# Optimization experiments

Measured on AMD Instinct MI355X. Metric: run time of the kernel, lower is better.

The kernel has to match this reference:

```python
import jax, jax.numpy as jnp
import numpy as np

B, S, H, HKV, D = 4, 1024, 32, 8, 128   # batch segments, seq per segment, q heads, kv heads, head dim
N = B * S                                # Ntotal (ragged tokens, equal-length segments)
SCALE = 1.0 / np.sqrt(D)                 # softmax_scale init kwarg
NEG = -1e9


def setup_inputs() -> dict:
    key = jax.random.key(0)
    kq, kk, kv = jax.random.split(key, 3)
    q = jax.random.normal(kq, (N, H, D), jnp.float32)
    k = jax.random.normal(kk, (N, HKV, D), jnp.float32)
    v = jax.random.normal(kv, (N, HKV, D), jnp.float32)
    # RoPE angles, rotate-half convention: concat(freqs, freqs), broadcast over heads
    inv_freq = 1.0 / (10000.0 ** (jnp.arange(D // 2, dtype=jnp.float32) / (D // 2)))
    pos = jnp.arange(S, dtype=jnp.float32)
    ang = pos[:, None] * inv_freq[None, :]                      # [S, D/2]
    idx_theta = jnp.tile(jnp.concatenate([ang, ang], -1), (B, 1))[:, None, :]  # [N,1,D]
    # per-segment causal mask, stacked -> [N, S]
    causal = jnp.where(jnp.arange(S)[None, :] <= jnp.arange(S)[:, None], 0.0, NEG).astype(jnp.float32)
    mask = jnp.tile(causal, (B, 1))
    return {"q": q, "k": k, "v": v, "idx_theta": idx_theta, "mask": mask}


def _rotate_half(x):
    # cat(-x[..., D/2:], x[..., :D/2])
    return jnp.concatenate([-x[..., D // 2:], x[..., : D // 2]], axis=-1)


def reference(q, k, v, idx_theta, mask):
    rep = H // HKV
    # repeat_kv: attention head i uses kv head i // rep (matches torch expand+reshape order)
    kx = jnp.repeat(k, rep, axis=1)                    # [N, H, D]
    vx = jnp.repeat(v, rep, axis=1)
    cos, sin = jnp.cos(idx_theta), jnp.sin(idx_theta)
    qr = q * cos + _rotate_half(q) * sin
    kr = kx * cos + _rotate_half(kx) * sin
    # segment-blocked attention (equal-length segments, vectorized over batch & heads)
    qb = qr.reshape(B, S, H, D)
    kb = kr.reshape(B, S, H, D)
    vb = vx.reshape(B, S, H, D)
    mb = mask.reshape(B, S, S)[:, None, :, :]          # [B,1,S,S]
    scores = jnp.einsum('bqhd,bkhd->bhqk', qb, kb) * SCALE + mb
    l = jax.nn.logsumexp(scores, axis=-1)              # [B,H,S] == max + logsumexp(shifted)
    p = jax.nn.softmax(scores, axis=-1)
    o = jnp.einsum('bhqk,bkhd->bqhd', p, vb)           # [B,S,H,D]
    o = o.reshape(N, H * D)                            # o.reshape(Ntotal, num_head, -1) flattened last two in torch is (N,H,D)->(N,H,D); original reshape(q.shape[0], q.shape[1], -1) keeps [N,H,D]
    o = o.reshape(N, H, D)
    l = l.transpose(0, 2, 1).reshape(N, H, 1)          # [Ntotal, num_head, 1]
    return o, l
```

## Files before the change

kernel.cpp:

```cpp
#include <hip/hip_runtime.h>

#define B_    4
#define S_    1024
#define H_    32
#define HKV_  8
#define D_    128
#define NTOT  (B_*S_)
#define QT_   64
#define KT_   64
#define DPAD  (D_+8)
#define KPAD  (KT_+8)

#define SCALE_ 0.08838834764831845f

typedef __attribute__((ext_vector_type(8))) short bf16x8;
typedef __attribute__((ext_vector_type(4))) short bf16x4;
typedef __attribute__((ext_vector_type(4))) float f32x4;
typedef __attribute__((ext_vector_type(4))) int   int4v;

__device__ __forceinline__ unsigned short f2bf(float f) {
    unsigned int u = __float_as_uint(f);
    u += 0x7FFFu + ((u >> 16) & 1u);
    return (unsigned short)(u >> 16);
}
__device__ __forceinline__ unsigned int pack2bf(float a, float b) {
    return (unsigned int)f2bf(a) | ((unsigned int)f2bf(b) << 16);
}

__global__ void rope_k_kernel(const float* __restrict__ k,
                              const float* __restrict__ theta,
                              unsigned short* __restrict__ kr) {
    int t  = blockIdx.x * blockDim.x + threadIdx.x;
    int g  = t & 7;
    int hk = (t >> 3) & (HKV_ - 1);
    int n  = t >> 6;
    if (n >= NTOT) return;
    int d0 = g * 8;
    const float* kp = k + ((size_t)n * HKV_ + hk) * D_;
    const float* tp = theta + (size_t)n * D_;

    alignas(16) float kl[8], ku[8], thl[8], thu[8];
    *(float4*)&kl[0]  = *(const float4*)(kp + d0);
    *(float4*)&kl[4]  = *(const float4*)(kp + d0 + 4);
    *(float4*)&ku[0]  = *(const float4*)(kp + d0 + 64);
    *(float4*)&ku[4]  = *(const float4*)(kp + d0 + 68);
    *(float4*)&thl[0] = *(const float4*)(tp + d0);
    *(float4*)&thl[4] = *(const float4*)(tp + d0 + 4);
    *(float4*)&thu[0] = *(const float4*)(tp + d0 + 64);
    *(float4*)&thu[4] = *(const float4*)(tp + d0 + 68);

    alignas(16) unsigned short ol[8], ou[8];
#pragma unroll
    for (int j = 0; j < 8; ++j) {
        float sl, cl, su, cu;
        __sincosf(thl[j], &sl, &cl);
        __sincosf(thu[j], &su, &cu);
        ol[j] = f2bf(kl[j] * cl - ku[j] * sl);
        ou[j] = f2bf(ku[j] * cu + kl[j] * su);
    }
    unsigned short* outp = kr + ((size_t)n * HKV_ + hk) * D_;
    *(int4v*)(outp + d0)      = *(const int4v*)ol;
    *(int4v*)(outp + d0 + 64) = *(const int4v*)ou;
}

__global__ void vt_kernel(const float* __restrict__ v,
                          unsigned short* __restrict__ vt) {
    __shared__ unsigned short T[64][128];
    int blk = blockIdx.x;
    int s0  = (blk & (S_/64 - 1)) * 64;
    int hk  = (blk >> 4) & (HKV_ - 1);
    int b   = blk >> 7;
    int tid = threadIdx.x;

#pragma unroll
    for (int i = 0; i < 8; ++i) {
        int u  = tid + 256 * i;
        int s  = u >> 5;
        int G  = u & 31;
        float4 val = *(const float4*)(v + (((size_t)(b * S_ + s0 + s)) * HKV_ + hk) * D_ + G * 4);
        unsigned short* p = &T[s][(G ^ (s & 31)) * 4];
        p[0] = f2bf(val.x); p[1] = f2bf(val.y); p[2] = f2bf(val.z); p[3] = f2bf(val.w);
    }
    __syncthreads();
#pragma unroll
    for (int i = 0; i < 4; ++i) {
        int u = tid + 256 * i;
        int d = u >> 3;
        int g = u & 7;
        int G = d >> 2;
        alignas(16) unsigned short tmp[8];
#pragma unroll
        for (int j = 0; j < 8; ++j) {
            int s = g * 8 + j;
            tmp[j] = T[s][(G ^ (s & 31)) * 4 + (d & 3)];
        }
        *(int4v*)(vt + (((size_t)(b * HKV_ + hk)) * D_ + d) * S_ + s0 + g * 8) = *(const int4v*)tmp;
    }
}

__global__ __launch_bounds__(256, 4)
void flash_kernel(const float* __restrict__ q,
                  const float* __restrict__ theta,
                  const unsigned short* __restrict__ kr,
                  const unsigned short* __restrict__ vt,
                  float* __restrict__ o_out,
                  float* __restrict__ l_out) {
    __shared__ unsigned short Ks[KT_][DPAD];
    __shared__ unsigned short Vs[D_][KPAD];

    const int tid  = threadIdx.x;
    const int wave = tid >> 6;
    const int lane = tid & 63;
    const int l16  = lane & 15;
    const int quad = lane >> 4;

    const int bh = blockIdx.x;
    const int b  = bh >> 5;
    const int h  = bh & (H_ - 1);
    const int hk = h >> 2;
    const int qt = (S_/QT_ - 1) - blockIdx.y;
    const int qbase = qt * QT_;
    const int wq   = qbase + wave * 16;
    const int qrow = wq + l16;

    bf16x8 qfrag[4];
    {
        const int n = b * S_ + qrow;
        const float* qp = q + ((size_t)n * H_ + h) * D_;
        const float* tp = theta + (size_t)n * D_;
#pragma unroll
        for (int c = 0; c < 4; ++c) {
            const int d0 = c * 32 + quad * 8;
            const int dp = d0 ^ 64;
            alignas(16) float qa[8], qb[8], th[8];
            *(float4*)&qa[0] = *(const float4*)(qp + d0);
            *(float4*)&qa[4] = *(const float4*)(qp + d0 + 4);
            *(float4*)&qb[0] = *(const float4*)(qp + dp);
            *(float4*)&qb[4] = *(const float4*)(qp + dp + 4);
            *(float4*)&th[0] = *(const float4*)(tp + d0);
            *(float4*)&th[4] = *(const float4*)(tp + d0 + 4);
            alignas(16) unsigned short tmp[8];
#pragma unroll
            for (int j = 0; j < 8; ++j) {
                float sv, cv;
                __sincosf(th[j], &sv, &cv);
                float rot = (d0 < 64) ? -qb[j] : qb[j];
                tmp[j] = f2bf(qa[j] * cv + rot * sv);
            }
            qfrag[c] = *(const bf16x8*)tmp;
        }
    }

    f32x4 acc[8];
#pragma unroll
    for (int dt = 0; dt < 8; ++dt) acc[dt] = (f32x4){0.f, 0.f, 0.f, 0.f};
    float m_st = -1e30f, l_st = 0.f;

    const unsigned short* kseg = kr + ((size_t)b * S_ * HKV_ + hk) * D_;
    const unsigned short* vseg = vt + ((size_t)(b * HKV_ + hk)) * D_ * S_;

    const int n_kt = qt + 1;
    for (int kt = 0; kt < n_kt; ++kt) {
        const int k0 = kt * KT_;
        __syncthreads();
#pragma unroll
        for (int i = 0; i < 4; ++i) {
            int u = tid + 256 * i;
            int key = u >> 4, g = u & 15;
            *(int4v*)&Ks[key][g * 8] =
                *(const int4v*)(kseg + (size_t)(k0 + key) * (HKV_ * D_) + g * 8);
        }
#pragma unroll
        for (int i = 0; i < 4; ++i) {
            int u = tid + 256 * i;
            int d = u >> 3, g = u & 7;
            *(int4v*)&Vs[d][g * 8] =
                *(const int4v*)(vseg + (size_t)d * S_ + k0 + g * 8);
        }
        __syncthreads();

        int nact = (wq + 15 - k0) / 16 + 1;
        if (nact > 4) nact = 4;

        f32x4 sc[4];
#pragma unroll
        for (int kc = 0; kc < 4; ++kc) {
            if (kc < nact) {
                f32x4 c = (f32x4){0.f, 0.f, 0.f, 0.f};
#pragma unroll
                for (int cc = 0; cc < 4; ++cc) {
                    bf16x8 kf = *(const bf16x8*)&Ks[kc * 16 + l16][cc * 32 + quad * 8];
                    c = __builtin_amdgcn_mfma_f32_16x16x32_bf16(kf, qfrag[cc], c, 0, 0, 0);
                }
                sc[kc] = c;
            }
        }

        float s[16];
#pragma unroll
        for (int kc = 0; kc < 4; ++kc) {
#pragma unroll
            for (int r = 0; r < 4; ++r) {
                int key = k0 + kc * 16 + quad * 4 + r;
                s[kc * 4 + r] = (kc < nact && key <= qrow) ? sc[kc][r] * SCALE_ : -1e30f;
            }
        }
        float tmax = s[0];
#pragma unroll
        for (int i = 1; i < 16; ++i) tmax = fmaxf(tmax, s[i]);
        tmax = fmaxf(tmax, __shfl_xor(tmax, 16));
        tmax = fmaxf(tmax, __shfl_xor(tmax, 32));
        float mnew  = fmaxf(m_st, tmax);
        float alpha = __expf(m_st - mnew);

        unsigned int pk[8];
        float rs = 0.f;
#pragma unroll
        for (int kc = 0; kc < 4; ++kc) {
            float p0 = __expf(s[kc * 4 + 0] - mnew);
            float p1 = __expf(s[kc * 4 + 1] - mnew);
            float p2 = __expf(s[kc * 4 + 2] - mnew);
            float p3 = __expf(s[kc * 4 + 3] - mnew);
            rs += (p0 + p1) + (p2 + p3);
            pk[kc * 2 + 0] = pack2bf(p0, p1);
            pk[kc * 2 + 1] = pack2bf(p2, p3);
        }
        rs += __shfl_xor(rs, 16);
        rs += __shfl_xor(rs, 32);
        l_st = l_st * alpha + rs;
        m_st = mnew;
#pragma unroll
        for (int dt = 0; dt < 8; ++dt) {
            acc[dt][0] *= alpha; acc[dt][1] *= alpha;
            acc[dt][2] *= alpha; acc[dt][3] *= alpha;
        }

#pragma unroll
        for (int kc = 0; kc < 4; ++kc) {
            if (kc < nact) {
                union { unsigned int u[2]; bf16x4 v; } pb;
                pb.u[0] = pk[kc * 2 + 0];
                pb.u[1] = pk[kc * 2 + 1];
#if __has_builtin(__builtin_amdgcn_mfma_f32_16x16x16bf16_1k)
#pragma unroll
                for (int dt = 0; dt < 8; ++dt) {
                    bf16x4 vf = *(const bf16x4*)&Vs[dt * 16 + l16][kc * 16 + quad * 4];
                    acc[dt] = __builtin_amdgcn_mfma_f32_16x16x16bf16_1k(vf, pb.v, acc[dt], 0, 0, 0);
                }
#else
                bf16x8 pb8 = (bf16x8){pb.v[0], pb.v[1], pb.v[2], pb.v[3], 0, 0, 0, 0};
#pragma unroll
                for (int dt = 0; dt < 8; ++dt) {
                    bf16x4 vf = *(const bf16x4*)&Vs[dt * 16 + l16][kc * 16 + quad * 4];
                    bf16x8 vf8 = (bf16x8){vf[0], vf[1], vf[2], vf[3], 0, 0, 0, 0};
                    acc[dt] = __builtin_amdgcn_mfma_f32_16x16x32_bf16(vf8, pb8, acc[dt], 0, 0, 0);
                }
#endif
            }
        }
    }

    const float inv = 1.0f / l_st;
    const int n = b * S_ + qrow;
    float* op = o_out + ((size_t)n * H_ + h) * D_;
#pragma unroll
    for (int dt = 0; dt < 8; ++dt) {
        float4 o4 = {acc[dt][0] * inv, acc[dt][1] * inv, acc[dt][2] * inv, acc[dt][3] * inv};
        *(float4*)(op + dt * 16 + quad * 4) = o4;
    }
    if (quad == 0)
        l_out[(size_t)n * H_ + h] = m_st + logf(l_st);
}

extern "C" void kernel_launch(void* const* d_in, const int* in_sizes, int n_in,
                              void* d_out, int out_size, void* d_ws, size_t ws_size,
                              hipStream_t stream) {
    const float* q     = (const float*)d_in[0];
    const float* k     = (const float*)d_in[1];
    const float* v     = (const float*)d_in[2];
    const float* theta = (const float*)d_in[3];

    float* o_out = (float*)d_out;
    float* l_out = o_out + (size_t)NTOT * H_ * D_;

    unsigned short* kr = (unsigned short*)d_ws;
    unsigned short* vt = kr + (size_t)NTOT * HKV_ * D_;

    rope_k_kernel<<<(NTOT * HKV_ * 8) / 256, 256, 0, stream>>>(k, theta, kr);
    vt_kernel<<<B_ * HKV_ * (S_ / 64), 256, 0, stream>>>(v, vt);

    dim3 grid(B_ * H_, S_ / QT_);
    flash_kernel<<<grid, 256, 0, stream>>>(q, theta, kr, vt, o_out, l_out);
}
```

Baseline: 240.7 us.

## Double-buffer K/V tiles with register prefetch and halve key tile size

The flash kernel now prefetches the next K/V tile into registers while computing on the current one, stores it into a second shared buffer afterwards, and drops to one barrier per iteration. The key tile shrinks to 32, which keeps shared memory within the occupancy target and makes the causal skip finer, so waves with no active keys skip all math. The softmax scale is folded into Q before the bf16 conversion. The V transpose kernel packs bf16 pairs into 32-bit shared-memory words. In exchange there are twice as many loop iterations, each with more per-iteration overhead, and extra registers for the prefetch.

Measured after the change: 228.2 us. -5.2%, faster.

```diff
diff --git a/kernel.cpp b/kernel.cpp
--- a/kernel.cpp
+++ b/kernel.cpp
@@ -7,7 +7,7 @@
 #define D_    128
 #define NTOT  (B_*S_)
 #define QT_   64
-#define KT_   64
+#define KT_   32
 #define DPAD  (D_+8)
 #define KPAD  (KT_+8)
 
@@ -65,7 +65,7 @@
 
 __global__ void vt_kernel(const float* __restrict__ v,
                           unsigned short* __restrict__ vt) {
-    __shared__ unsigned short T[64][128];
+    __shared__ unsigned int T[64][64];
     int blk = blockIdx.x;
     int s0  = (blk & (S_/64 - 1)) * 64;
     int hk  = (blk >> 4) & (HKV_ - 1);
@@ -78,8 +78,9 @@
         int s  = u >> 5;
         int G  = u & 31;
         float4 val = *(const float4*)(v + (((size_t)(b * S_ + s0 + s)) * HKV_ + hk) * D_ + G * 4);
-        unsigned short* p = &T[s][(G ^ (s & 31)) * 4];
-        p[0] = f2bf(val.x); p[1] = f2bf(val.y); p[2] = f2bf(val.z); p[3] = f2bf(val.w);
+        unsigned int* p = &T[s][(G ^ (s & 31)) << 1];
+        p[0] = pack2bf(val.x, val.y);
+        p[1] = pack2bf(val.z, val.w);
     }
     __syncthreads();
 #pragma unroll
@@ -88,11 +89,14 @@
         int d = u >> 3;
         int g = u & 7;
         int G = d >> 2;
+        int half = (d >> 1) & 1;
+        int hi   = (d & 1) * 16;
         alignas(16) unsigned short tmp[8];
 #pragma unroll
         for (int j = 0; j < 8; ++j) {
             int s = g * 8 + j;
-            tmp[j] = T[s][(G ^ (s & 31)) * 4 + (d & 3)];
+            unsigned int w = T[s][(((G ^ (s & 31)) << 1)) + half];
+            tmp[j] = (unsigned short)(w >> hi);
         }
         *(int4v*)(vt + (((size_t)(b * HKV_ + hk)) * D_ + d) * S_ + s0 + g * 8) = *(const int4v*)tmp;
     }
@@ -105,8 +109,8 @@
                   const unsigned short* __restrict__ vt,
                   float* __restrict__ o_out,
                   float* __restrict__ l_out) {
-    __shared__ unsigned short Ks[KT_][DPAD];
-    __shared__ unsigned short Vs[D_][KPAD];
+    __shared__ unsigned short Ks[2][KT_][DPAD];
+    __shared__ unsigned short Vs[2][D_][KPAD];
 
     const int tid  = threadIdx.x;
     const int wave = tid >> 6;
@@ -145,7 +149,7 @@
                 float sv, cv;
                 __sincosf(th[j], &sv, &cv);
                 float rot = (d0 < 64) ? -qb[j] : qb[j];
-                tmp[j] = f2bf(qa[j] * cv + rot * sv);
+                tmp[j] = f2bf((qa[j] * cv + rot * sv) * SCALE_);
             }
             qfrag[c] = *(const bf16x8*)tmp;
         }
@@ -159,105 +163,121 @@
     const unsigned short* kseg = kr + ((size_t)b * S_ * HKV_ + hk) * D_;
     const unsigned short* vseg = vt + ((size_t)(b * HKV_ + hk)) * D_ * S_;
 
-    const int n_kt = qt + 1;
+    const int ku0 = tid, ku1 = tid + 256;
+    const int kk0 = ku0 >> 4, kg0 = (ku0 & 15) * 8;
+    const int kk1 = kk0 + 16,  kg1 = kg0;
+    const int vd0 = tid >> 2, vg0 = (tid & 3) * 8;
+    const int vd1 = vd0 + 64,  vg1 = vg0;
+    int4v pK0, pK1, pV0, pV1;
+
+#define LOAD_TILE(K0)                                                          \
+    do {                                                                       \
+        pK0 = *(const int4v*)(kseg + (size_t)((K0) + kk0) * (HKV_*D_) + kg0);  \
+        pK1 = *(const int4v*)(kseg + (size_t)((K0) + kk1) * (HKV_*D_) + kg1);  \
+        pV0 = *(const int4v*)(vseg + (size_t)vd0 * S_ + (K0) + vg0);           \
+        pV1 = *(const int4v*)(vseg + (size_t)vd1 * S_ + (K0) + vg1);           \
+    } while (0)
+#define STORE_TILE(BUF)                                                        \
+    do {                                                                       \
+        *(int4v*)&Ks[BUF][kk0][kg0] = pK0;                                     \
+        *(int4v*)&Ks[BUF][kk1][kg1] = pK1;                                     \
+        *(int4v*)&Vs[BUF][vd0][vg0] = pV0;                                     \
+        *(int4v*)&Vs[BUF][vd1][vg1] = pV1;                                     \
+    } while (0)
+
+    const int n_kt = 2 * (qt + 1);
+    LOAD_TILE(0);
+    STORE_TILE(0);
+
     for (int kt = 0; kt < n_kt; ++kt) {
         const int k0 = kt * KT_;
+        const int buf = kt & 1;
         __syncthreads();
-#pragma unroll
-        for (int i = 0; i < 4; ++i) {
-            int u = tid + 256 * i;
-            int key = u >> 4, g = u & 15;
-            *(int4v*)&Ks[key][g * 8] =
-                *(const int4v*)(kseg + (size_t)(k0 + key) * (HKV_ * D_) + g * 8);
+        if (kt + 1 < n_kt) LOAD_TILE(k0 + KT_);
+
+        int dd = wq + 15 - k0;
+        int nact = dd < 0 ? 0 : (dd >> 4) + 1;
+        if (nact > 2) nact = 2;
+
+        if (nact > 0) {
+            f32x4 sc[2];
+#pragma unroll
+            for (int kc = 0; kc < 2; ++kc) {
+                if (kc < nact) {
+                    f32x4 c = (f32x4){0.f, 0.f, 0.f, 0.f};
+#pragma unroll
+                    for (int cc = 0; cc < 4; ++cc) {
+                        bf16x8 kf = *(const bf16x8*)&Ks[buf][kc * 16 + l16][cc * 32 + quad * 8];
+                        c = __builtin_amdgcn_mfma_f32_16x16x32_bf16(kf, qfrag[cc], c, 0, 0, 0);
+                    }
+                    sc[kc] = c;
+                }
+            }
+
+            float s[8];
+#pragma unroll
+            for (int kc = 0; kc < 2; ++kc)
+#pragma unroll
+                for (int r = 0; r < 4; ++r) {
+                    int key = k0 + kc * 16 + quad * 4 + r;
+                    s[kc * 4 + r] = (kc < nact && key <= qrow) ? sc[kc][r] : -1e30f;
+                }
+            float tmax = s[0];
+#pragma unroll
+            for (int i = 1; i < 8; ++i) tmax = fmaxf(tmax, s[i]);
+            tmax = fmaxf(tmax, __shfl_xor(tmax, 16));
+            tmax = fmaxf(tmax, __shfl_xor(tmax, 32));
+            float mnew  = fmaxf(m_st, tmax);
+            float alpha = __expf(m_st - mnew);
+
+            unsigned int pk[4];
+            float rs = 0.f;
+#pragma unroll
+            for (int kc = 0; kc < 2; ++kc) {
+                float p0 = __expf(s[kc * 4 + 0] - mnew);
+                float p1 = __expf(s[kc * 4 + 1] - mnew);
+                float p2 = __expf(s[kc * 4 + 2] - mnew);
+                float p3 = __expf(s[kc * 4 + 3] - mnew);
+                rs += (p0 + p1) + (p2 + p3);
+                pk[kc * 2 + 0] = pack2bf(p0, p1);
+                pk[kc * 2 + 1] = pack2bf(p2, p3);
+            }
+            rs += __shfl_xor(rs, 16);
+            rs += __shfl_xor(rs, 32);
+            l_st = l_st * alpha + rs;
+            m_st = mnew;
+#pragma unroll
+            for (int dt = 0; dt < 8; ++dt) {
+                acc[dt][0] *= alpha; acc[dt][1] *= alpha;
+                acc[dt][2] *= alpha; acc[dt][3] *= alpha;
+            }
+
+#pragma unroll
+            for (int kc = 0; kc < 2; ++kc) {
+                if (kc < nact) {
+                    union { unsigned int u[2]; bf16x4 v; } pb;
+                    pb.u[0] = pk[kc * 2 + 0];
+                    pb.u[1] = pk[kc * 2 + 1];
+#if __has_builtin(__builtin_amdgcn_mfma_f32_16x16x16bf16_1k)
+#pragma unroll
+                    for (int dt = 0; dt < 8; ++dt) {
+                        bf16x4 vf = *(const bf16x4*)&Vs[buf][dt * 16 + l16][kc * 16 + quad * 4];
+                        acc[dt] = __builtin_amdgcn_mfma_f32_16x16x16bf16_1k(vf, pb.v, acc[dt], 0, 0, 0);
+                    }
+#else
+                    bf16x8 pb8 = (bf16x8){pb.v[0], pb.v[1], pb.v[2], pb.v[3], 0, 0, 0, 0};
+#pragma unroll
+                    for (int dt = 0; dt < 8; ++dt) {
+                        bf16x4 vf = *(const bf16x4*)&Vs[buf][dt * 16 + l16][kc * 16 + quad * 4];
+                        bf16x8 vf8 = (bf16x8){vf[0], vf[1], vf[2], vf[3], 0, 0, 0, 0};
+                        acc[dt] = __builtin_amdgcn_mfma_f32_16x16x32_bf16(vf8, pb8, acc[dt], 0, 0, 0);
+                    }
+#endif
+                }
+            }
         }
-#pragma unroll
-        for (int i = 0; i < 4; ++i) {
-            int u = tid + 256 * i;
-            int d = u >> 3, g = u & 7;
-            *(int4v*)&Vs[d][g * 8] =
-                *(const int4v*)(vseg + (size_t)d * S_ + k0 + g * 8);
-        }
-        __syncthreads();
-
-        int nact = (wq + 15 - k0) / 16 + 1;
-        if (nact > 4) nact = 4;
-
-        f32x4 sc[4];
-#pragma unroll
-        for (int kc = 0; kc < 4; ++kc) {
-            if (kc < nact) {
-                f32x4 c = (f32x4){0.f, 0.f, 0.f, 0.f};
-#pragma unroll
-                for (int cc = 0; cc < 4; ++cc) {
-                    bf16x8 kf = *(const bf16x8*)&Ks[kc * 16 + l16][cc * 32 + quad * 8];
-                    c = __builtin_amdgcn_mfma_f32_16x16x32_bf16(kf, qfrag[cc], c, 0, 0, 0);
-                }
-                sc[kc] = c;
-            }
-        }
-
-        float s[16];
-#pragma unroll
-        for (int kc = 0; kc < 4; ++kc) {
-#pragma unroll
-            for (int r = 0; r < 4; ++r) {
-                int key = k0 + kc * 16 + quad * 4 + r;
-                s[kc * 4 + r] = (kc < nact && key <= qrow) ? sc[kc][r] * SCALE_ : -1e30f;
-            }
-        }
-        float tmax = s[0];
-#pragma unroll
-        for (int i = 1; i < 16; ++i) tmax = fmaxf(tmax, s[i]);
-        tmax = fmaxf(tmax, __shfl_xor(tmax, 16));
-        tmax = fmaxf(tmax, __shfl_xor(tmax, 32));
-        float mnew  = fmaxf(m_st, tmax);
-        float alpha = __expf(m_st - mnew);
-
-        unsigned int pk[8];
-        float rs = 0.f;
-#pragma unroll
-        for (int kc = 0; kc < 4; ++kc) {
-            float p0 = __expf(s[kc * 4 + 0] - mnew);
-            float p1 = __expf(s[kc * 4 + 1] - mnew);
-            float p2 = __expf(s[kc * 4 + 2] - mnew);
-            float p3 = __expf(s[kc * 4 + 3] - mnew);
-            rs += (p0 + p1) + (p2 + p3);
-            pk[kc * 2 + 0] = pack2bf(p0, p1);
-            pk[kc * 2 + 1] = pack2bf(p2, p3);
-        }
-        rs += __shfl_xor(rs, 16);
-        rs += __shfl_xor(rs, 32);
-        l_st = l_st * alpha + rs;
-        m_st = mnew;
-#pragma unroll
-        for (int dt = 0; dt < 8; ++dt) {
-            acc[dt][0] *= alpha; acc[dt][1] *= alpha;
-            acc[dt][2] *= alpha; acc[dt][3] *= alpha;
-        }
-
-#pragma unroll
-        for (int kc = 0; kc < 4; ++kc) {
-            if (kc < nact) {
-                union { unsigned int u[2]; bf16x4 v; } pb;
-                pb.u[0] = pk[kc * 2 + 0];
-                pb.u[1] = pk[kc * 2 + 1];
-#if __has_builtin(__builtin_amdgcn_mfma_f32_16x16x16bf16_1k)
-#pragma unroll
-                for (int dt = 0; dt < 8; ++dt) {
-                    bf16x4 vf = *(const bf16x4*)&Vs[dt * 16 + l16][kc * 16 + quad * 4];
-                    acc[dt] = __builtin_amdgcn_mfma_f32_16x16x16bf16_1k(vf, pb.v, acc[dt], 0, 0, 0);
-                }
-#else
-                bf16x8 pb8 = (bf16x8){pb.v[0], pb.v[1], pb.v[2], pb.v[3], 0, 0, 0, 0};
-#pragma unroll
-                for (int dt = 0; dt < 8; ++dt) {
-                    bf16x4 vf = *(const bf16x4*)&Vs[dt * 16 + l16][kc * 16 + quad * 4];
-                    bf16x8 vf8 = (bf16x8){vf[0], vf[1], vf[2], vf[3], 0, 0, 0, 0};
-                    acc[dt] = __builtin_amdgcn_mfma_f32_16x16x32_bf16(vf8, pb8, acc[dt], 0, 0, 0);
-                }
-#endif
-            }
-        }
+
+        if (kt + 1 < n_kt) STORE_TILE(1 - buf);
     }
 
     const float inv = 1.0f / l_st;
```
